# Optimization experiments

Measured on AMD Instinct MI355X. Metric: run time of the kernel, lower is better.

The kernel has to match this reference:

```python
import jax, jax.numpy as jnp
import numpy as np

RHO = 1060.0   # blood density kg/m^3
DX = 1e-3      # grid spacing
CCFL = 0.9     # CFL number
EPS_A = 1e-6   # area floor


def setup_inputs() -> dict:
    key = jax.random.key(0)
    k0, k1, k2 = jax.random.split(key, 3)
    M = 90000          # 3 vessels x 30000 cells
    T = 150            # time steps
    Rs = jax.random.normal(k0, (4,), dtype=jnp.float32)
    sim_dat = jnp.ones((2, M), dtype=jnp.float32)            # row0: A, row1: Q seed
    sim_dat_const = jax.random.uniform(k1, (11, M), dtype=jnp.float32)
    input_data = jax.random.uniform(k2, (T,), dtype=jnp.float32)
    strides = jnp.array([[0, 30000], [30000, 60000], [60000, 90000]], dtype=jnp.int32)
    return {"Rs": Rs, "sim_dat": sim_dat, "sim_dat_const": sim_dat_const,
            "input_data": input_data, "strides": strides, "upper": T}


def reference(Rs, sim_dat, sim_dat_const, input_data, strides, upper):
    M = sim_dat.shape[1]
    # --- SimDense: softplus reparam of 4 resistance scale factors ---
    rs = jax.nn.softplus(Rs)
    idx = jnp.arange(M)
    m1 = (idx >= strides[1, 0]) & (idx < strides[1, 1])  # vessel 1 region
    m2 = (idx >= strides[2, 0]) & (idx < strides[2, 1])  # vessel 2 region
    # constant rows (shifted positive)
    A0 = sim_dat_const[0] + 0.5     # reference area
    beta = sim_dat_const[1] + 1.0   # wall stiffness
    R1 = sim_dat_const[7] + 0.5     # proximal resistance (VAR_INDEX_1)
    R2 = sim_dat_const[8] + 0.5     # distal resistance (VAR_INDEX_2)
    # scatter scaled resistances into vessel-1 / vessel-2 regions
    R1 = jnp.where(m1, rs[0] * R1, jnp.where(m2, rs[2] * R1, R1))
    R2 = jnp.where(m1, rs[1] * R2, jnp.where(m2, rs[3] * R2, R2))
    Rtot = R1 + R2

    A_init = sim_dat[0]
    Q_init = 0.1 * sim_dat[1]
    starts = strides[:, 0]
    ends = strides[:, 1] - 1
    mids = (strides[:, 0] + strides[:, 1]) // 2

    def step(carry, inflow):
        A, Q = carry
        A = jnp.maximum(A, EPS_A)
        sq = jnp.sqrt(A / A0)
        P = beta * (sq - 1.0)                 # tube-law pressure
        u = Q / A
        c = jnp.sqrt(0.5 * beta / RHO * sq)   # wave speed
        smax = jnp.max(jnp.abs(u) + c)
        dt = CCFL * DX / smax                 # CFL-limited timestep
        # conservative fluxes for (A, Q)
        F_A = Q
        F_Q = Q * u + beta / (3.0 * RHO * A0) * A * sq
        # Lax-Friedrichs interface fluxes
        fhA = 0.5 * (F_A[:-1] + F_A[1:]) - 0.5 * smax * (A[1:] - A[:-1])
        fhQ = 0.5 * (F_Q[:-1] + F_Q[1:]) - 0.5 * smax * (Q[1:] - Q[:-1])
        lam = dt / DX
        A_new = A.at[1:-1].add(-lam * (fhA[1:] - fhA[:-1]))
        Q_new = Q.at[1:-1].add(-lam * (fhQ[1:] - fhQ[:-1]))
        # inlet / junction BC: prescribed inflow at each vessel start
        Q_new = Q_new.at[starts].set(inflow)
        # outlet BC: resistive Windkessel Q = P / (R1 + R2)
        Q_new = Q_new.at[ends].set(P[ends] / Rtot[ends])
        A_new = jnp.maximum(A_new, EPS_A)
        return (A_new, Q_new), P[mids]          # record mid-vessel pressures

    _, p = jax.lax.scan(step, (A_init, Q_init), input_data)
    return p  # [upper, 3]
```

## Files before the change

### kernel.cpp

```cpp
#include <hip/hip_runtime.h>

static constexpr int MM  = 90000;
static constexpr int TT  = 150;
static constexpr int BS  = 256;
static constexpr int CPT = 4;
static constexpr int CPB = BS * CPT;
static constexpr int NB  = (MM + CPB - 1) / CPB;
static constexpr int WPB = BS / 64;
static constexpr int NWAVE = NB * WPB;
static constexpr int WPAGES = 384;
static constexpr int PAGE_U32 = 2048;
static constexpr int PAGE_U64 = 1024;
static constexpr int GUARD_MAX = 4096;

typedef unsigned int u32x2 __attribute__((ext_vector_type(2)));

__device__ __attribute__((aligned(128))) unsigned int       g_wmax[WPAGES][PAGE_U32];
__device__ __attribute__((aligned(128))) unsigned long long g_edge_s[NB][PAGE_U64];
__device__ unsigned long long g_dummy64;

__device__ __forceinline__ float softplus_f(float x) {
    return fmaxf(x, 0.0f) + log1pf(expf(-fabsf(x)));
}
__device__ __forceinline__ unsigned long long packAQ(float A, float Q) {
    return ((unsigned long long)__float_as_uint(Q) << 32) | (unsigned long long)__float_as_uint(A);
}
#define AG_STORE32(p, v) __hip_atomic_store((p), (v), __ATOMIC_RELAXED, __HIP_MEMORY_SCOPE_AGENT)
#define AG_STORE64(p, v) __hip_atomic_store((p), (v), __ATOMIC_RELAXED, __HIP_MEMORY_SCOPE_AGENT)

#define ISSUE7(x0,x1,x2,x3,x4,x5,e,p0,p1,p2,p3,p4,p5,pe)                        \
    asm volatile("global_load_dword %0, %7, off sc1\n\t"                        \
                 "global_load_dword %1, %8, off sc1\n\t"                        \
                 "global_load_dword %2, %9, off sc1\n\t"                        \
                 "global_load_dword %3, %10, off sc1\n\t"                       \
                 "global_load_dword %4, %11, off sc1\n\t"                       \
                 "global_load_dword %5, %12, off sc1\n\t"                       \
                 "global_load_dwordx2 %6, %13, off sc1"                         \
                 : "=&v"(x0),"=&v"(x1),"=&v"(x2),"=&v"(x3),"=&v"(x4),"=&v"(x5),"=&v"(e) \
                 : "v"(p0),"v"(p1),"v"(p2),"v"(p3),"v"(p4),"v"(p5),"v"(pe)      \
                 : "memory")
#define WAIT7_TIE(x0,x1,x2,x3,x4,x5,e)                                          \
    do { asm volatile("s_waitcnt vmcnt(7)"                                      \
             : "+v"(x0),"+v"(x1),"+v"(x2),"+v"(x3),"+v"(x4),"+v"(x5),"+v"(e)    \
             :: "memory");                                                      \
         __builtin_amdgcn_sched_barrier(0); } while (0)
#define CHK7(x0,x1,x2,x3,x4,x5,e)                                               \
    __all(((x0) != 0u) & ((x1) != 0u) & ((x2) != 0u) & ((x3) != 0u) &           \
          ((x4) != 0u) & ((x5) != 0u) & ((e).x != 0u))
#define FENCE_LDS() asm volatile("s_waitcnt lgkmcnt(0)" ::: "memory")
#define BAR() do { FENCE_LDS();                                                 \
                   __builtin_amdgcn_s_barrier();                                \
                   __builtin_amdgcn_sched_barrier(0); } while (0)

#define DPP_MAX(x, ctrl, rm, bm)                                                \
    x = fmaxf(x, __int_as_float(__builtin_amdgcn_update_dpp(                    \
                     0, __float_as_int(x), (ctrl), (rm), (bm), true)))
__device__ __forceinline__ float wave_max64(float x) {
    DPP_MAX(x, 0x111, 0xf, 0xf);
    DPP_MAX(x, 0x112, 0xf, 0xf);
    DPP_MAX(x, 0x114, 0xf, 0xe);
    DPP_MAX(x, 0x118, 0xf, 0xc);
    DPP_MAX(x, 0x142, 0xa, 0xf);
    DPP_MAX(x, 0x143, 0xc, 0xf);
    return x;
}

__global__ void init_ws_kernel() {
    int i = blockIdx.x * blockDim.x + threadIdx.x;
    int stride = gridDim.x * blockDim.x;
    unsigned int* pw = &g_wmax[0][0];
    for (int j = i; j < WPAGES * PAGE_U32; j += stride)
        pw[j] = ((j >> 11) < NWAVE) ? 0u : 1u;
    unsigned long long* pe = &g_edge_s[0][0];
    for (int j = i; j < NB * PAGE_U64; j += stride) pe[j] = 0ull;
    if (i == 0) g_dummy64 = ~0ull;
}

__global__ void __launch_bounds__(BS) sim_kernel(
    const float* __restrict__ Rs,
    const float* __restrict__ sim_dat,
    const float* __restrict__ sdc,
    const float* __restrict__ inflow,
    float* __restrict__ out)
{
    __shared__ float sE[2][WPB][2][3];
    __shared__ float s_smaxv;
    __shared__ float s_hL[3], s_hR[3];
    __shared__ float s_inflow[TT];
    __shared__ int   s_panic;

    const int b    = blockIdx.x;
    const int tid  = threadIdx.x;
    const int wv   = tid >> 6;
    const int lane = tid & 63;
    const int base = b * CPB + tid * CPT;
    const int gw   = b * WPB + wv;

    for (int j = tid; j < TT; j += BS) s_inflow[j] = inflow[j];
    if (tid == 0) s_panic = 0;

    float A[CPT], Q[CPT], A0v[CPT], bet[CPT], cbv[CPT], k2v[CPT], sq[CPT], FQ[CPT];
    bool  act[CPT];
    #pragma unroll
    for (int c = 0; c < CPT; ++c) {
        int i = base + c;
        act[c] = (i < MM);
        if (act[c]) {
            A[c]   = fmaxf(sim_dat[i], 1e-6f);
            Q[c]   = 0.1f * sim_dat[MM + i];
            A0v[c] = sdc[i] + 0.5f;
            bet[c] = sdc[MM + i] + 1.0f;
        } else { A[c] = 1.0f; Q[c] = 0.0f; A0v[c] = 1.0f; bet[c] = 1.0f; }
        cbv[c] = (0.5f * bet[c]) / 1060.0f;
        k2v[c] = bet[c] / (3180.0f * A0v[c]);
    }
    const bool isStart = (base == 0) | (base == 30000) | (base == 60000);
    const bool isEnd   = (base + 3 == 29999) | (base + 3 == 59999) | (base + 3 == 89999);
    const int midSlot = (base == 15000) ? 0 : (base == 45000) ? 1 : (base == 75000) ? 2 : -1;
    float Rtot = 1.0f;
    if (isEnd) {
        int i3 = base + 3;
        float R1 = sdc[7 * MM + i3] + 0.5f;
        float R2 = sdc[8 * MM + i3] + 0.5f;
        if (i3 == 59999)      { R1 *= softplus_f(Rs[0]); R2 *= softplus_f(Rs[1]); }
        else if (i3 == 89999) { R1 *= softplus_f(Rs[2]); R2 *= softplus_f(Rs[3]); }
        Rtot = R1 + R2;
    }

    const bool pubL = (tid == 0) && (b > 0);
    const bool pubR = (tid == BS - 1) && (b < NB - 1);

    float s4 = 0.0f;
    #pragma unroll
    for (int c = 0; c < CPT; ++c) {
        sq[c] = sqrtf(A[c] / A0v[c]);
        float uu = Q[c] / A[c];
        float cc = sqrtf(cbv[c] * sq[c]);
        FQ[c] = Q[c] * uu + k2v[c] * A[c] * sq[c];
        s4 = fmaxf(s4, act[c] ? (fabsf(uu) + cc) : 0.0f);
    }
    if (pubL) {
        AG_STORE64(&g_edge_s[b][0], packAQ(A[0], Q[0]));
        AG_STORE64(&g_edge_s[b][1], (unsigned long long)__float_as_uint(FQ[0]));
    }
    if (pubR) {
        AG_STORE64(&g_edge_s[b][2], packAQ(A[3], Q[3]));
        AG_STORE64(&g_edge_s[b][3], (unsigned long long)__float_as_uint(FQ[3]));
    }
    {
        float red = wave_max64(s4);
        if (lane == 63) AG_STORE32(&g_wmax[gw][0], __float_as_uint(red));
    }
    if (lane == 0)       { sE[0][wv][0][0] = A[0]; sE[0][wv][0][1] = Q[0]; sE[0][wv][0][2] = FQ[0]; }
    else if (lane == 63) { sE[0][wv][1][0] = A[3]; sE[0][wv][1][1] = Q[3]; sE[0][wv][1][2] = FQ[3]; }

    for (int t = 0; t < TT; ++t) {
        const int par = t & 1, npar = par ^ 1;

        unsigned int b0, b1, b2, b3, b4, b5, c0, c1, c2, c3, c4, c5;
        u32x2 bE, cE;
        const unsigned int *p0, *p1, *p2, *p3, *p4, *p5;
        const unsigned long long* pE;
        if (wv == 0) {
            p0 = &g_wmax[lane      ][t];  p1 = &g_wmax[lane +  64][t];
            p2 = &g_wmax[lane + 128][t];  p3 = &g_wmax[lane + 192][t];
            p4 = &g_wmax[lane + 256][t];  p5 = &g_wmax[lane + 320][t];
            const int t4 = t * 4;
            pE = &g_dummy64;
            if (lane == 0 && b > 0)           pE = &g_edge_s[b - 1][t4 + 2];
            else if (lane == 1 && b > 0)      pE = &g_edge_s[b - 1][t4 + 3];
            else if (lane == 2 && b < NB - 1) pE = &g_edge_s[b + 1][t4 + 0];
            else if (lane == 3 && b < NB - 1) pE = &g_edge_s[b + 1][t4 + 1];
            ISSUE7(b0, b1, b2, b3, b4, b5, bE, p0, p1, p2, p3, p4, p5, pE);
        }

        float Am = __shfl_up(A[3], 1, 64),  Qm = __shfl_up(Q[3], 1, 64),  Fm = __shfl_up(FQ[3], 1, 64);
        float Ap = __shfl_down(A[0], 1, 64), Qp = __shfl_down(Q[0], 1, 64), Fp = __shfl_down(FQ[0], 1, 64);

        float dFA[CPT], lapA[CPT], dFQ[CPT], lapQ[CPT];
        #pragma unroll
        for (int c = 0; c < CPT; ++c) {
            float Al = (c == 0) ? Am : A[c-1],  Ql = (c == 0) ? Qm : Q[c-1],  Fl = (c == 0) ? Fm : FQ[c-1];
            float Ar = (c == 3) ? Ap : A[c+1],  Qr = (c == 3) ? Qp : Q[c+1],  Fr = (c == 3) ? Fp : FQ[c+1];
            dFA[c]  = 0.5f * (Qr - Ql);
            lapA[c] = 0.5f * (Ar - 2.0f * A[c] + Al);
            dFQ[c]  = 0.5f * (Fr - Fl);
            lapQ[c] = 0.5f * (Qr - 2.0f * Q[c] + Ql);
        }
        if (midSlot >= 0) out[t * 3 + midSlot] = bet[0] * (sq[0] - 1.0f);
        float qFix = 0.0f;
        if (isStart) qFix = s_inflow[t];
        if (isEnd)   qFix = (bet[3] * (sq[3] - 1.0f)) / Rtot;

        if (wv == 0) {
            ISSUE7(c0, c1, c2, c3, c4, c5, cE, p0, p1, p2, p3, p4, p5, pE);
            WAIT7_TIE(b0, b1, b2, b3, b4, b5, bE);
            if (!CHK7(b0, b1, b2, b3, b4, b5, bE)) {
                int guard = 0;
                for (;;) {
                    ISSUE7(b0, b1, b2, b3, b4, b5, bE, p0, p1, p2, p3, p4, p5, pE);
                    WAIT7_TIE(c0, c1, c2, c3, c4, c5, cE);
                    if (CHK7(c0, c1, c2, c3, c4, c5, cE)) {
                        b0=c0; b1=c1; b2=c2; b3=c3; b4=c4; b5=c5; bE=cE; break;
                    }
                    ISSUE7(c0, c1, c2, c3, c4, c5, cE, p0, p1, p2, p3, p4, p5, pE);
                    WAIT7_TIE(b0, b1, b2, b3, b4, b5, bE);
                    if (CHK7(b0, b1, b2, b3, b4, b5, bE)) break;
                    if (++guard >= GUARD_MAX) { if (lane == 0) s_panic = 1; break; }
                }
            }
            if (lane == 0 && b > 0)           { s_hL[0] = __uint_as_float(bE.x);
                                                s_hL[1] = __uint_as_float(bE.y); }
            else if (lane == 1 && b > 0)      { s_hL[2] = __uint_as_float(bE.x); }
            else if (lane == 2 && b < NB - 1) { s_hR[0] = __uint_as_float(bE.x);
                                                s_hR[1] = __uint_as_float(bE.y); }
            else if (lane == 3 && b < NB - 1) { s_hR[2] = __uint_as_float(bE.x); }
            float m = fmaxf(fmaxf(fmaxf(__uint_as_float(b0), __uint_as_float(b1)),
                                  fmaxf(__uint_as_float(b2), __uint_as_float(b3))),
                            fmaxf(__uint_as_float(b4), __uint_as_float(b5)));
            m = wave_max64(m);
            if (lane == 63) s_smaxv = __int_as_float(__builtin_amdgcn_readlane(__float_as_int(m), 63));
        }
        BAR();
        if (s_panic) break;
        const float smax = s_smaxv;
        const float dt  = ((float)(0.9 * 0.001)) / smax;
        const float lam = dt / 0.001f;
        const float w   = lam * smax;

        if (lane == 0 && (wv > 0 || b > 0)) {
            float Al, Ql, Fl;
            if (wv > 0) { Al = sE[par][wv-1][1][0]; Ql = sE[par][wv-1][1][1]; Fl = sE[par][wv-1][1][2]; }
            else        { Al = s_hL[0];             Ql = s_hL[1];             Fl = s_hL[2]; }
            dFA[0]  = 0.5f * (Q[1] - Ql);
            lapA[0] = 0.5f * (A[1] - 2.0f * A[0] + Al);
            dFQ[0]  = 0.5f * (FQ[1] - Fl);
            lapQ[0] = 0.5f * (Q[1] - 2.0f * Q[0] + Ql);
        }
        if (lane == 63 && (wv < WPB - 1 || b < NB - 1)) {
            float Ar, Qr, Fr;
            if (wv < WPB - 1) { Ar = sE[par][wv+1][0][0]; Qr = sE[par][wv+1][0][1]; Fr = sE[par][wv+1][0][2]; }
            else              { Ar = s_hR[0];             Qr = s_hR[1];             Fr = s_hR[2]; }
            dFA[3]  = 0.5f * (Qr - Q[2]);
            lapA[3] = 0.5f * (Ar - 2.0f * A[3] + A[2]);
            dFQ[3]  = 0.5f * (Fr - FQ[2]);
            lapQ[3] = 0.5f * (Qr - 2.0f * Q[3] + Q[2]);
        }

        #pragma unroll
        for (int c = 0; c < CPT; ++c) {
            int i = base + c;
            if (act[c] && i > 0 && i < MM - 1) {
                A[c] = fmaf(w, lapA[c], fmaf(-lam, dFA[c], A[c]));
                Q[c] = fmaf(w, lapQ[c], fmaf(-lam, dFQ[c], Q[c]));
            }
        }
        if (isStart) Q[0] = qFix;
        if (isEnd)   Q[3] = qFix;
        #pragma unroll
        for (int c = 0; c < CPT; ++c) A[c] = fmaxf(A[c], 1e-6f);

        const int n4 = (t + 1) * 4;
        if (pubL) AG_STORE64(&g_edge_s[b][n4 + 0], packAQ(A[0], Q[0]));
        if (pubR) AG_STORE64(&g_edge_s[b][n4 + 2], packAQ(A[3], Q[3]));

        float uu[CPT];
        s4 = 0.0f;
        #pragma unroll
        for (int c = 0; c < CPT; ++c) {
            sq[c] = sqrtf(A[c] / A0v[c]);
            uu[c] = Q[c] / A[c];
            float cc = sqrtf(cbv[c] * sq[c]);
            s4 = fmaxf(s4, act[c] ? (fabsf(uu[c]) + cc) : 0.0f);
        }
        {
            float red = wave_max64(s4);
            if (lane == 63) AG_STORE32(&g_wmax[gw][t + 1], __float_as_uint(red));
        }
        #pragma unroll
        for (int c = 0; c < CPT; ++c)
            FQ[c] = Q[c] * uu[c] + k2v[c] * A[c] * sq[c];

        if (pubL) AG_STORE64(&g_edge_s[b][n4 + 1], (unsigned long long)__float_as_uint(FQ[0]));
        if (pubR) AG_STORE64(&g_edge_s[b][n4 + 3], (unsigned long long)__float_as_uint(FQ[3]));

        if (lane == 0)       { sE[npar][wv][0][0] = A[0]; sE[npar][wv][0][1] = Q[0]; sE[npar][wv][0][2] = FQ[0]; }
        else if (lane == 63) { sE[npar][wv][1][0] = A[3]; sE[npar][wv][1][1] = Q[3]; sE[npar][wv][1][2] = FQ[3]; }
    }
}

extern "C" void kernel_launch(void* const* d_in, const int* in_sizes, int n_in,
                              void* d_out, int out_size, void* d_ws, size_t ws_size,
                              hipStream_t stream) {
    (void)in_sizes; (void)n_in; (void)d_ws; (void)ws_size; (void)out_size;

    const float* Rs      = (const float*)d_in[0];
    const float* sim_dat = (const float*)d_in[1];
    const float* sdc     = (const float*)d_in[2];
    const float* inflow  = (const float*)d_in[3];
    float* out = (float*)d_out;

    hipLaunchKernelGGL(init_ws_kernel, dim3(240), dim3(256), 0, stream);

    hipLaunchKernelGGL(sim_kernel, dim3(NB), dim3(BS), 0, stream,
                       Rs, sim_dat, sdc, inflow, out);
}
```

Baseline: 464.1 us.

## Replace per-step block barrier with LDS flag broadcast of lam/w

Drops the per-timestep workgroup barrier. Wave 0 now computes lam and w and publishes them as a packed 64-bit word in a per-step LDS slot, and the other waves spin on that slot. Edge-value LDS writes are moved ahead of the global wmax store and guarded with an lgkmcnt fence, so neighbour waves see them before the step can complete. The edge flux computation is also reordered so the global edge stores are issued earlier. The aim is to cut barrier stalls on the grid-wide critical path, at the cost of LDS spin-polling and subtler memory-ordering assumptions between waves.

```diff
diff --git a/kernel.cpp b/kernel.cpp
--- a/kernel.cpp
+++ b/kernel.cpp
@@ -48,9 +48,6 @@
     __all(((x0) != 0u) & ((x1) != 0u) & ((x2) != 0u) & ((x3) != 0u) &           \
           ((x4) != 0u) & ((x5) != 0u) & ((e).x != 0u))
 #define FENCE_LDS() asm volatile("s_waitcnt lgkmcnt(0)" ::: "memory")
-#define BAR() do { FENCE_LDS();                                                 \
-                   __builtin_amdgcn_s_barrier();                                \
-                   __builtin_amdgcn_sched_barrier(0); } while (0)
 
 #define DPP_MAX(x, ctrl, rm, bm)                                                \
     x = fmaxf(x, __int_as_float(__builtin_amdgcn_update_dpp(                    \
@@ -84,7 +81,7 @@
     float* __restrict__ out)
 {
     __shared__ float sE[2][WPB][2][3];
-    __shared__ float s_smaxv;
+    __shared__ unsigned long long s_lamw[TT];
     __shared__ float s_hL[3], s_hR[3];
     __shared__ float s_inflow[TT];
     __shared__ int   s_panic;
@@ -96,7 +93,7 @@
     const int base = b * CPB + tid * CPT;
     const int gw   = b * WPB + wv;
 
-    for (int j = tid; j < TT; j += BS) s_inflow[j] = inflow[j];
+    for (int j = tid; j < TT; j += BS) { s_inflow[j] = inflow[j]; s_lamw[j] = 0ull; }
     if (tid == 0) s_panic = 0;
 
     float A[CPT], Q[CPT], A0v[CPT], bet[CPT], cbv[CPT], k2v[CPT], sq[CPT], FQ[CPT];
@@ -147,12 +144,14 @@
         AG_STORE64(&g_edge_s[b][2], packAQ(A[3], Q[3]));
         AG_STORE64(&g_edge_s[b][3], (unsigned long long)__float_as_uint(FQ[3]));
     }
+    if (lane == 0)       { sE[0][wv][0][0] = A[0]; sE[0][wv][0][1] = Q[0]; sE[0][wv][0][2] = FQ[0]; }
+    else if (lane == 63) { sE[0][wv][1][0] = A[3]; sE[0][wv][1][1] = Q[3]; sE[0][wv][1][2] = FQ[3]; }
     {
         float red = wave_max64(s4);
+        FENCE_LDS();
         if (lane == 63) AG_STORE32(&g_wmax[gw][0], __float_as_uint(red));
     }
-    if (lane == 0)       { sE[0][wv][0][0] = A[0]; sE[0][wv][0][1] = Q[0]; sE[0][wv][0][2] = FQ[0]; }
-    else if (lane == 63) { sE[0][wv][1][0] = A[3]; sE[0][wv][1][1] = Q[3]; sE[0][wv][1][2] = FQ[3]; }
+    __syncthreads();
 
     for (int t = 0; t < TT; ++t) {
         const int par = t & 1, npar = par ^ 1;
@@ -192,6 +191,7 @@
         if (isStart) qFix = s_inflow[t];
         if (isEnd)   qFix = (bet[3] * (sq[3] - 1.0f)) / Rtot;
 
+        float lam, w;
         if (wv == 0) {
             ISSUE7(c0, c1, c2, c3, c4, c5, cE, p0, p1, p2, p3, p4, p5, pE);
             WAIT7_TIE(b0, b1, b2, b3, b4, b5, bE);
@@ -219,14 +219,24 @@
                                   fmaxf(__uint_as_float(b2), __uint_as_float(b3))),
                             fmaxf(__uint_as_float(b4), __uint_as_float(b5)));
             m = wave_max64(m);
-            if (lane == 63) s_smaxv = __int_as_float(__builtin_amdgcn_readlane(__float_as_int(m), 63));
-        }
-        BAR();
-        if (s_panic) break;
-        const float smax = s_smaxv;
-        const float dt  = ((float)(0.9 * 0.001)) / smax;
-        const float lam = dt / 0.001f;
-        const float w   = lam * smax;
+            const float smax = __int_as_float(__builtin_amdgcn_readlane(__float_as_int(m), 63));
+            const float dt = ((float)(0.9 * 0.001)) / smax;
+            lam = dt / 0.001f;
+            w   = lam * smax;
+            FENCE_LDS();
+            if (lane == 0) {
+                *(volatile unsigned long long*)&s_lamw[t] =
+                    ((unsigned long long)__float_as_uint(w) << 32)
+                    | (unsigned long long)__float_as_uint(lam);
+            }
+        } else {
+            const volatile unsigned long long* vf = (const volatile unsigned long long*)&s_lamw[t];
+            unsigned long long lw;
+            do { lw = *vf; } while ((unsigned int)lw == 0u);
+            lam = __uint_as_float((unsigned int)lw);
+            w   = __uint_as_float((unsigned int)(lw >> 32));
+        }
+        if (*(volatile int*)&s_panic) break;
 
         if (lane == 0 && (wv > 0 || b > 0)) {
             float Al, Ql, Fl;
@@ -265,27 +275,30 @@
         if (pubR) AG_STORE64(&g_edge_s[b][n4 + 2], packAQ(A[3], Q[3]));
 
         float uu[CPT];
+        sq[0] = sqrtf(A[0] / A0v[0]);  uu[0] = Q[0] / A[0];
+        sq[3] = sqrtf(A[3] / A0v[3]);  uu[3] = Q[3] / A[3];
+        FQ[0] = Q[0] * uu[0] + k2v[0] * A[0] * sq[0];
+        FQ[3] = Q[3] * uu[3] + k2v[3] * A[3] * sq[3];
+        if (pubL) AG_STORE64(&g_edge_s[b][n4 + 1], (unsigned long long)__float_as_uint(FQ[0]));
+        if (pubR) AG_STORE64(&g_edge_s[b][n4 + 3], (unsigned long long)__float_as_uint(FQ[3]));
+        sq[1] = sqrtf(A[1] / A0v[1]);  uu[1] = Q[1] / A[1];
+        sq[2] = sqrtf(A[2] / A0v[2]);  uu[2] = Q[2] / A[2];
+        FQ[1] = Q[1] * uu[1] + k2v[1] * A[1] * sq[1];
+        FQ[2] = Q[2] * uu[2] + k2v[2] * A[2] * sq[2];
         s4 = 0.0f;
         #pragma unroll
         for (int c = 0; c < CPT; ++c) {
-            sq[c] = sqrtf(A[c] / A0v[c]);
-            uu[c] = Q[c] / A[c];
             float cc = sqrtf(cbv[c] * sq[c]);
             s4 = fmaxf(s4, act[c] ? (fabsf(uu[c]) + cc) : 0.0f);
         }
+
+        if (lane == 0)       { sE[npar][wv][0][0] = A[0]; sE[npar][wv][0][1] = Q[0]; sE[npar][wv][0][2] = FQ[0]; }
+        else if (lane == 63) { sE[npar][wv][1][0] = A[3]; sE[npar][wv][1][1] = Q[3]; sE[npar][wv][1][2] = FQ[3]; }
         {
             float red = wave_max64(s4);
+            FENCE_LDS();
             if (lane == 63) AG_STORE32(&g_wmax[gw][t + 1], __float_as_uint(red));
         }
-        #pragma unroll
-        for (int c = 0; c < CPT; ++c)
-            FQ[c] = Q[c] * uu[c] + k2v[c] * A[c] * sq[c];
-
-        if (pubL) AG_STORE64(&g_edge_s[b][n4 + 1], (unsigned long long)__float_as_uint(FQ[0]));
-        if (pubR) AG_STORE64(&g_edge_s[b][n4 + 3], (unsigned long long)__float_as_uint(FQ[3]));
-
-        if (lane == 0)       { sE[npar][wv][0][0] = A[0]; sE[npar][wv][0][1] = Q[0]; sE[npar][wv][0][2] = FQ[0]; }
-        else if (lane == 63) { sE[npar][wv][1][0] = A[3]; sE[npar][wv][1][1] = Q[3]; sE[npar][wv][1][2] = FQ[3]; }
     }
 }
 
```

New measurement: 793.7 us. 71.0% more time.
